# Kernel optimization log

Hardware: AMD Instinct MI355X
Metric: run time of the kernel (lower is better)

## Reference

```python
import jax, jax.numpy as jnp
import numpy as np

L_LAYERS = 4
D_MODEL = 512
NHEAD = 8
HEAD_DIM = D_MODEL // NHEAD  # 64
DFF = 2048
N_TGT = 1024
N_MEM = 2048
BATCH = 2
EPS = 1e-5


def setup_inputs() -> dict:
    key = jax.random.key(0)
    ks = jax.random.split(key, 16)
    sc = 0.02  # small init so deep residual stack stays numerically sane
    inp = dict(
        tgt=jax.random.normal(ks[0], (N_TGT, BATCH, D_MODEL), jnp.float32),
        memory=jax.random.normal(ks[1], (N_MEM, BATCH, D_MODEL), jnp.float32),
        query_pos=jax.random.normal(ks[2], (N_TGT, BATCH, D_MODEL), jnp.float32),
        pos=jax.random.normal(ks[3], (N_MEM, BATCH, D_MODEL), jnp.float32),
        # per-layer stacked parameters (leading axis = layer)
        in_proj_w=jax.random.normal(ks[4], (L_LAYERS, 3 * D_MODEL, D_MODEL), jnp.float32) * sc,
        in_proj_b=jnp.zeros((L_LAYERS, 3 * D_MODEL), jnp.float32),
        out_w=jax.random.normal(ks[5], (L_LAYERS, D_MODEL, D_MODEL), jnp.float32) * sc,
        out_b=jnp.zeros((L_LAYERS, D_MODEL), jnp.float32),
        conv_w=jax.random.normal(ks[6], (L_LAYERS, 3, D_MODEL, D_MODEL), jnp.float32) * sc,  # Conv1d k=1 == matmul
        conv_b=jnp.zeros((L_LAYERS, 3, D_MODEL), jnp.float32),
        mlp_w=jax.random.normal(ks[7], (L_LAYERS, 1, HEAD_DIM), jnp.float32) * sc,  # down_mlp Linear(head_dim,1)
        mlp_b=jnp.zeros((L_LAYERS, 1), jnp.float32),
        lin1_w=jax.random.normal(ks[8], (L_LAYERS, DFF, D_MODEL), jnp.float32) * sc,
        lin1_b=jnp.zeros((L_LAYERS, DFF), jnp.float32),
        lin2_w=jax.random.normal(ks[9], (L_LAYERS, D_MODEL, DFF), jnp.float32) * sc,
        lin2_b=jnp.zeros((L_LAYERS, D_MODEL), jnp.float32),
        ln_g=jnp.ones((L_LAYERS, 3, D_MODEL), jnp.float32),
        ln_b=jnp.zeros((L_LAYERS, 3, D_MODEL), jnp.float32),
        final_g=jnp.ones((D_MODEL,), jnp.float32),
        final_b=jnp.zeros((D_MODEL,), jnp.float32),
    )
    return inp


def _layer_norm(x, g, b):
    m = jnp.mean(x, axis=-1, keepdims=True)
    v = jnp.mean(jnp.square(x - m), axis=-1, keepdims=True)
    return (x - m) * jax.lax.rsqrt(v + EPS) * g + b


def _mha(q_in, k_in, v_in, w, b, ow, ob):
    # standard torch nn.MultiheadAttention, inputs [L, B, D]
    wq, wk, wv = jnp.split(w, 3, axis=0)
    bq, bk, bv = jnp.split(b, 3)

    def heads(x, W, bb):  # [L,B,D] -> [B,H,L,hd]
        y = x @ W.T + bb
        return y.reshape(y.shape[0], BATCH, NHEAD, HEAD_DIM).transpose(1, 2, 0, 3)

    qh = heads(q_in, wq, bq)
    kh = heads(k_in, wk, bk)
    vh = heads(v_in, wv, bv)
    scores = jnp.einsum('bhnd,bhmd->bhnm', qh, kh) / np.sqrt(HEAD_DIM).astype(np.float32)
    prob = jax.nn.softmax(scores, axis=-1)
    o = jnp.einsum('bhnm,bhmd->bhnd', prob, vh)
    o = o.transpose(2, 0, 1, 3).reshape(-1, BATCH, D_MODEL)  # [N,B,D]
    return o @ ow.T + ob


def _custom_attn(q_nbd, k_nbd, v_nbd, cw, cb, mw, mb):
    # MultiHeadedAttention: Conv1d(k=1) projections then key-modulated scores.
    def prep(x, W, bb):  # [L,B,D] -> [B, head_dim, H, L]  (reshape splits D into (head_dim, H))
        y = jnp.einsum('od,bdl->bol', W, x.transpose(1, 2, 0)) + bb[None, :, None]
        return y.reshape(BATCH, HEAD_DIM, NHEAD, -1)

    q = prep(q_nbd, cw[0], cb[0])  # [B,hd,H,N]
    k = prep(k_nbd, cw[1], cb[1])  # [B,hd,H,M]
    v = prep(v_nbd, cw[2], cb[2])  # [B,hd,H,M]
    # scores_1 = einsum('bdhn,bdhm->bhnm', q, k)/sqrt(hd); scores_2 = einsum('abcd,aced->abcd', k, scores_1)
    # = k[b,d,h,m] * sum_n scores_1[b,h,n,m]. Fuse the n-sum (same math, avoids [B,H,N,M]).
    s1sum = jnp.einsum('bdh,bdhm->bhm', q.sum(axis=3), k) / np.sqrt(HEAD_DIM).astype(np.float32)
    s2 = k * s1sum[:, None, :, :]            # [B,hd,H,M]
    prob = jax.nn.softmax(s2, axis=-1)       # softmax over M
    x = jnp.einsum('bnhm,bdhm->bdhn', prob, v)  # [B,hd,H,hd]
    x = jnp.einsum('bdhn,on->bdho', x, mw) + mb  # down_mlp -> [B,hd,H,1]
    return x.reshape(BATCH, D_MODEL, -1).transpose(2, 0, 1)  # [1,B,D], broadcasts on residual add


def _decoder_layer(tgt, memory, query_pos, pos, ipw, ipb, ow, ob, cw, cb, mw, mb,
                   l1w, l1b, l2w, l2b, lng, lnb):
    q = tgt + query_pos
    t2 = _mha(q, q, tgt, ipw, ipb, ow, ob)
    tgt = _layer_norm(tgt + t2, lng[0], lnb[0])
    t2 = _custom_attn(tgt + query_pos, memory + pos, memory, cw, cb, mw, mb)
    tgt = _layer_norm(tgt + t2, lng[1], lnb[1])
    h = jax.nn.relu(tgt @ l1w.T + l1b)
    t2 = h @ l2w.T + l2b
    tgt = _layer_norm(tgt + t2, lng[2], lnb[2])
    return tgt


def reference(tgt, memory, query_pos, pos, in_proj_w, in_proj_b, out_w, out_b,
              conv_w, conv_b, mlp_w, mlp_b, lin1_w, lin1_b, lin2_w, lin2_b,
              ln_g, ln_b, final_g, final_b):
    out = tgt
    for i in range(L_LAYERS):
        out = _decoder_layer(out, memory, query_pos, pos,
                             in_proj_w[i], in_proj_b[i], out_w[i], out_b[i],
                             conv_w[i], conv_b[i], mlp_w[i], mlp_b[i],
                             lin1_w[i], lin1_b[i], lin2_w[i], lin2_b[i],
                             ln_g[i], ln_b[i])
    out = _layer_norm(out, final_g, final_b)
    return out[None]  # Decoder returns output.unsqueeze(0): [1, N, B, D]
```

## Files before the change

kernel.cpp:

```cpp
#include <hip/hip_runtime.h>
#include <cstdint>

typedef __attribute__((ext_vector_type(8))) short short8;
typedef __attribute__((ext_vector_type(4))) float f32x4;
typedef __attribute__((ext_vector_type(4))) unsigned short us4;
typedef unsigned short u16;

static __device__ __forceinline__ u16 f2bf(float f) {
  union { float f; unsigned u; } x; x.f = f;
  return (u16)((x.u + 0x7FFFu + ((x.u >> 16) & 1u)) >> 16);
}

static __device__ __forceinline__ float wred_max(float v) {
#pragma unroll
  for (int o = 32; o > 0; o >>= 1) v = fmaxf(v, __shfl_xor(v, o, 64));
  return v;
}
static __device__ __forceinline__ float wred_sum(float v) {
#pragma unroll
  for (int o = 32; o > 0; o >>= 1) v += __shfl_xor(v, o, 64);
  return v;
}

static __device__ __forceinline__ void gload16(const void* g, void* l) {
  __builtin_amdgcn_global_load_lds(
      (const __attribute__((address_space(1))) unsigned int*)g,
      (__attribute__((address_space(3))) unsigned int*)l, 16, 0, 0);
}

struct GemmP {
  const u16* A; const u16* B; void* C; const float* bias;
  int M, N, K, lda, ldb, crs, ccs;
  int azi, bzi, czi, biasdz;
  long aso, asi, bso, bsi, cso, csi, biassz;
  float scale; int relu; int cbf16;
};

template<int ROWS>
static __device__ __forceinline__ void stage_t(const u16* g, int ld, u16* lds,
                                               int w, int lane) {
#pragma unroll
  for (int j = 0; j < ROWS / 32; ++j) {
    const int idx = w * (ROWS / 32) + j;
    const int r = idx * 8 + (lane >> 3);
    const int gc = ((lane & 7) ^ (r & 7)) * 8;
    gload16(g + (long)r * ld + gc, lds + idx * 512);
  }
}

template<int BM, int BN>
__global__ __launch_bounds__(256, 4) void gemm_k(GemmP p) {
  constexpr int WTM = BM / 2, WTN = BN / 2;
  constexpr int FM = WTM / 16, FN = WTN / 16;
  __shared__ __align__(16) u16 Al[2][BM * 64];
  __shared__ __align__(16) u16 Bl[2][BN * 64];
  const int tid = threadIdx.x, lane = tid & 63, w = tid >> 6;
  const int wr = w >> 1, wc = w & 1, lr = lane & 15, lk4 = lane >> 4;
  const int z = blockIdx.z;
  const int tm = blockIdx.y * BM, tn = blockIdx.x * BN;
  const long ab = (long)(z / p.azi) * p.aso + (long)(z % p.azi) * p.asi + (long)tm * p.lda;
  const long bb = (long)(z / p.bzi) * p.bso + (long)(z % p.bzi) * p.bsi + (long)tn * p.ldb;
  const long cb = (long)(z / p.czi) * p.cso + (long)(z % p.czi) * p.csi;
  const long boff = p.biasdz ? (long)(z / p.biasdz) * p.biassz : 0;

  f32x4 acc[FM][FN];
#pragma unroll
  for (int i = 0; i < FM; ++i)
#pragma unroll
    for (int j = 0; j < FN; ++j) acc[i][j] = (f32x4)(0.0f);

  const u16* Ag = p.A + ab;
  const u16* Bg = p.B + bb;
  stage_t<BM>(Ag, p.lda, &Al[0][0], w, lane);
  stage_t<BN>(Bg, p.ldb, &Bl[0][0], w, lane);
  __syncthreads();

  const int nt = p.K >> 6;
  for (int t = 0; t < nt; ++t) {
    const int cur = t & 1;
    if (t + 1 < nt) {
      stage_t<BM>(Ag + (long)(t + 1) * 64, p.lda, &Al[cur ^ 1][0], w, lane);
      stage_t<BN>(Bg + (long)(t + 1) * 64, p.ldb, &Bl[cur ^ 1][0], w, lane);
    }
    short8 af[FM][2], bfv[FN][2];
#pragma unroll
    for (int ks = 0; ks < 2; ++ks) {
#pragma unroll
      for (int mi = 0; mi < FM; ++mi) {
        const int row = wr * WTM + mi * 16 + lr;
        const int off = row * 128 + ((ks * 4 + lk4) ^ (row & 7)) * 16;
        af[mi][ks] = *(const short8*)((const char*)&Al[cur][0] + off);
      }
#pragma unroll
      for (int ni = 0; ni < FN; ++ni) {
        const int row = wc * WTN + ni * 16 + lr;
        const int off = row * 128 + ((ks * 4 + lk4) ^ (row & 7)) * 16;
        bfv[ni][ks] = *(const short8*)((const char*)&Bl[cur][0] + off);
      }
    }
#pragma unroll
    for (int ks = 0; ks < 2; ++ks)
#pragma unroll
      for (int mi = 0; mi < FM; ++mi)
#pragma unroll
        for (int ni = 0; ni < FN; ++ni)
          acc[mi][ni] = __builtin_amdgcn_mfma_f32_16x16x32_bf16(af[mi][ks], bfv[ni][ks],
                                                                acc[mi][ni], 0, 0, 0);
    __syncthreads();
  }

  const int kg = lk4 * 4;
#pragma unroll
  for (int ni = 0; ni < FN; ++ni) {
    const int col = tn + wc * WTN + ni * 16 + lr;
    const float bv = p.bias ? p.bias[boff + col] : 0.0f;
#pragma unroll
    for (int mi = 0; mi < FM; ++mi) {
      const int rb = tm + wr * WTM + mi * 16 + kg;
#pragma unroll
      for (int r = 0; r < 4; ++r) {
        float v = acc[mi][ni][r] * p.scale + bv;
        if (p.relu) v = fmaxf(v, 0.0f);
        const long ci = cb + (long)(rb + r) * p.crs + (long)col * p.ccs;
        if (p.cbf16) ((u16*)p.C)[ci] = f2bf(v);
        else ((float*)p.C)[ci] = v;
      }
    }
  }
}

template<int BM, int BN>
static inline void launchg(const GemmP& p, int nb, hipStream_t s) {
  dim3 g((unsigned)(p.N / BN), (unsigned)(p.M / BM), (unsigned)nb);
  hipLaunchKernelGGL((gemm_k<BM, BN>), g, dim3(256), 0, s, p);
}

__global__ __launch_bounds__(256) void flash_attn(const u16* qkb, const u16* Vtb, u16* aob) {
  const int zh = blockIdx.x, b = zh >> 3, h = zh & 7;
  const int qt = blockIdx.y;
  const int tid = threadIdx.x, lane = tid & 63, w = tid >> 6;
  const int lr = lane & 15, g = lane >> 4;

  __shared__ __align__(16) u16 Kl[2][64 * 64];
  __shared__ __align__(16) u16 Vl[2][64 * 64];
  __shared__ __align__(16) u16 Pl[4][16 * 64];

  const int nrow = qt * 64 + w * 16 + lr;
  const long qbase = ((long)(nrow * 2 + b)) * 1024 + h * 64;
  const short8 q0 = *(const short8*)&qkb[qbase + g * 8];
  const short8 q1 = *(const short8*)&qkb[qbase + 32 + g * 8];

  f32x4 acc_o[4];
#pragma unroll
  for (int i = 0; i < 4; ++i) acc_o[i] = (f32x4)(0.0f);
  float m_run = -3e38f, l_run = 0.0f;

  auto stage = [&](int buf, int t) {
    const int m0 = t * 64;
#pragma unroll
    for (int j = 0; j < 2; ++j) {
      const int c = w * 2 + j;
      const int row = c * 8 + (lane >> 3);
      const int src = (lane & 7) ^ (row & 7);
      gload16(qkb + ((long)((m0 + row) * 2 + b)) * 1024 + 512 + h * 64 + src * 8,
              &Kl[buf][c * 512]);
      gload16(Vtb + (long)b * 524288 + ((long)(h * 64 + row)) * 1024 + m0 + src * 8,
              &Vl[buf][c * 512]);
    }
  };

  stage(0, 0);
  __syncthreads();

  for (int t = 0; t < 16; ++t) {
    const int cur = t & 1;
    if (t < 15) stage(cur ^ 1, t + 1);

    f32x4 s_acc[4];
#pragma unroll
    for (int ks = 0; ks < 4; ++ks) {
      const int krow = ks * 16 + lr;
      const short8 k0 = *(const short8*)&Kl[cur][krow * 64 + ((g ^ (krow & 7)) * 8)];
      const short8 k1 = *(const short8*)&Kl[cur][krow * 64 + (((4 + g) ^ (krow & 7)) * 8)];
      f32x4 z4 = (f32x4)(0.0f);
      z4 = __builtin_amdgcn_mfma_f32_16x16x32_bf16(k0, q0, z4, 0, 0, 0);
      z4 = __builtin_amdgcn_mfma_f32_16x16x32_bf16(k1, q1, z4, 0, 0, 0);
      s_acc[ks] = z4;
    }

    float mx = -3e38f;
#pragma unroll
    for (int ks = 0; ks < 4; ++ks)
#pragma unroll
      for (int r = 0; r < 4; ++r) mx = fmaxf(mx, s_acc[ks][r]);
    mx = fmaxf(mx, __shfl_xor(mx, 16, 64));
    mx = fmaxf(mx, __shfl_xor(mx, 32, 64));
    mx *= 0.125f;
    const float m_new = fmaxf(m_run, mx);
    const float alpha = __expf(m_run - m_new);
    float psum = 0.0f;
    u16 pb[4][4];
#pragma unroll
    for (int ks = 0; ks < 4; ++ks)
#pragma unroll
      for (int r = 0; r < 4; ++r) {
        const float pv = __expf(s_acc[ks][r] * 0.125f - m_new);
        psum += pv;
        pb[ks][r] = f2bf(pv);
      }
    psum += __shfl_xor(psum, 16, 64);
    psum += __shfl_xor(psum, 32, 64);
    l_run = l_run * alpha + psum;
    m_run = m_new;
#pragma unroll
    for (int i = 0; i < 4; ++i) acc_o[i] *= alpha;

#pragma unroll
    for (int ks = 0; ks < 4; ++ks)
#pragma unroll
      for (int r = 0; r < 4; ++r) {
        const int m = ks * 16 + g * 4 + r;
        Pl[w][lr * 64 + (((m >> 3) ^ (lr & 7)) * 8) + (m & 7)] = pb[ks][r];
      }

#pragma unroll
    for (int mh = 0; mh < 2; ++mh) {
      const short8 pt = *(const short8*)&Pl[w][lr * 64 + (((mh * 4 + g) ^ (lr & 7)) * 8)];
#pragma unroll
      for (int ds = 0; ds < 4; ++ds) {
        const int drow = ds * 16 + lr;
        const short8 vt = *(const short8*)&Vl[cur][drow * 64 + (((mh * 4 + g) ^ (drow & 7)) * 8)];
        acc_o[ds] = __builtin_amdgcn_mfma_f32_16x16x32_bf16(vt, pt, acc_o[ds], 0, 0, 0);
      }
    }
    __syncthreads();
  }

  const float invl = 1.0f / l_run;
#pragma unroll
  for (int ds = 0; ds < 4; ++ds)
#pragma unroll
    for (int r = 0; r < 4; ++r) {
      const int d = ds * 16 + g * 4 + r;
      aob[((long)(nrow * 2 + b)) * 512 + h * 64 + d] = f2bf(acc_o[ds][r] * invl);
    }
}

__global__ __launch_bounds__(256) void ln512(const float* a, const float* res, int resmode,
                                             const float* g, const float* bt,
                                             float* out, u16* obf,
                                             const float* add2, u16* obf2) {
  const int row = blockIdx.x * 4 + (threadIdx.x >> 6);
  const int lane = threadIdx.x & 63;
  const float* ar = a + (long)row * 512;
  f32x4 x[2];
#pragma unroll
  for (int i = 0; i < 2; ++i) {
    const int idx = (i * 64 + lane) * 4;
    x[i] = *(const f32x4*)&ar[idx];
    if (resmode == 1) x[i] += *(const f32x4*)&res[(long)row * 512 + idx];
    else if (resmode == 2) x[i] += *(const f32x4*)&res[(row & 1) * 512 + idx];
  }
  float s = 0.f;
#pragma unroll
  for (int i = 0; i < 2; ++i)
#pragma unroll
    for (int j = 0; j < 4; ++j) s += x[i][j];
  const float mean = wred_sum(s) * (1.0f / 512.0f);
  float vv = 0.f;
#pragma unroll
  for (int i = 0; i < 2; ++i)
#pragma unroll
    for (int j = 0; j < 4; ++j) { const float d = x[i][j] - mean; vv += d * d; }
  vv = wred_sum(vv) * (1.0f / 512.0f);
  const float rs = rsqrtf(vv + 1e-5f);
#pragma unroll
  for (int i = 0; i < 2; ++i) {
    const int idx = (i * 64 + lane) * 4;
    const f32x4 gv = *(const f32x4*)&g[idx];
    const f32x4 bv = *(const f32x4*)&bt[idx];
    f32x4 o;
#pragma unroll
    for (int j = 0; j < 4; ++j) o[j] = (x[i][j] - mean) * rs * gv[j] + bv[j];
    *(f32x4*)&out[(long)row * 512 + idx] = o;
    if (obf) {
      us4 ov;
#pragma unroll
      for (int j = 0; j < 4; ++j) ov[j] = f2bf(o[j]);
      *(us4*)&obf[(long)row * 512 + idx] = ov;
    }
    if (obf2) {
      const f32x4 a2 = *(const f32x4*)&add2[(long)row * 512 + idx];
      us4 ov;
#pragma unroll
      for (int j = 0; j < 4; ++j) ov[j] = f2bf(o[j] + a2[j]);
      *(us4*)&obf2[(long)row * 512 + idx] = ov;
    }
  }
}

struct CvtSeg { const float* s; u16* d; int nblk; };
struct Cvt5 { CvtSeg seg[5]; };
__global__ __launch_bounds__(256) void cvt_multi(Cvt5 c) {
  int b = blockIdx.x, si = 0;
  while (si < 4 && b >= c.seg[si].nblk) { b -= c.seg[si].nblk; ++si; }
  const float* a = c.seg[si].s;
  u16* o = c.seg[si].d;
  const long i = ((long)b * 256 + threadIdx.x) * 8;
  f32x4 a0 = *(const f32x4*)&a[i], a1 = *(const f32x4*)&a[i + 4];
  short8 ov;
#pragma unroll
  for (int k = 0; k < 4; ++k) { ov[k] = (short)f2bf(a0[k]); ov[k + 4] = (short)f2bf(a1[k]); }
  *(short8*)&o[i] = ov;
}

__global__ __launch_bounds__(256) void cvt2(const float* a, const float* b, u16* oa, u16* oab) {
  const long i = ((long)blockIdx.x * 256 + threadIdx.x) * 8;
  f32x4 a0 = *(const f32x4*)&a[i], a1 = *(const f32x4*)&a[i + 4];
  f32x4 b0 = *(const f32x4*)&b[i], b1 = *(const f32x4*)&b[i + 4];
  short8 o1, o2;
#pragma unroll
  for (int c = 0; c < 4; ++c) {
    o1[c] = (short)f2bf(a0[c]); o1[c + 4] = (short)f2bf(a1[c]);
    o2[c] = (short)f2bf(a0[c] + b0[c]); o2[c + 4] = (short)f2bf(a1[c] + b1[c]);
  }
  *(short8*)&oa[i] = o1; *(short8*)&oab[i] = o2;
}

__global__ __launch_bounds__(512) void xsum1(const float* x1, const float* qpos, float* xp) {
  const int b = blockIdx.x >> 4, c = blockIdx.x & 15, d = threadIdx.x;
  float a = 0.f;
  for (int n = c * 64; n < c * 64 + 64; ++n) {
    const long i = ((long)(n * 2 + b)) * 512 + d;
    a += x1[i] + qpos[i];
  }
  xp[blockIdx.x * 512 + d] = a;
}

__global__ __launch_bounds__(512) void xsum2(const float* xp, float* xs) {
  const int b = blockIdx.x, d = threadIdx.x;
  float a = 0.f;
#pragma unroll
  for (int c = 0; c < 16; ++c) a += xp[(b * 16 + c) * 512 + d];
  xs[b * 512 + d] = a;
}

__global__ __launch_bounds__(256) void s1_k(const float* xs, const float* W0, const float* b0,
                                            const float* kT, float* s1) {
  const int z = blockIdx.x, b = z >> 3, h = z & 7;
  const int tid = threadIdx.x;
  __shared__ float part[4][64];
  __shared__ float qs[64];
  const int d = tid & 63, qd = tid >> 6;
  const int ch = d * 8 + h;
  float pp = 0.f;
  const float* wrp = W0 + (long)ch * 512 + qd * 128;
  const float* xrp = xs + b * 512 + qd * 128;
#pragma unroll 8
  for (int i = 0; i < 128; ++i) pp += wrp[i] * xrp[i];
  part[qd][d] = pp;
  __syncthreads();
  if (tid < 64)
    qs[tid] = part[0][tid] + part[1][tid] + part[2][tid] + part[3][tid]
              + 1024.0f * b0[tid * 8 + h];
  __syncthreads();
  const int m = blockIdx.y * 256 + tid;
  float a = 0.f;
#pragma unroll 8
  for (int dd = 0; dd < 64; ++dd)
    a += qs[dd] * kT[((long)b * 512 + dd * 8 + h) * 2048 + m];
  s1[(long)z * 2048 + m] = 0.125f * a;
}

__global__ __launch_bounds__(256) void pw_k(const float* kT, const float* s1,
                                            const float* mw, float* pwpart) {
  const int z = blockIdx.x & 15, c = blockIdx.x >> 4;
  const int b = z >> 3, h = z & 7;
  const int tid = threadIdx.x, lane = tid & 63, wid = tid >> 6;
  __shared__ float redm[4], reds[4];
  float s1v[8], pwa[8];
#pragma unroll
  for (int i = 0; i < 8; ++i) { s1v[i] = s1[(long)z * 2048 + tid + i * 256]; pwa[i] = 0.f; }
  for (int n = c * 8; n < c * 8 + 8; ++n) {
    const float* kr = kT + ((long)b * 512 + n * 8 + h) * 2048;
    float sv[8];
    float mx = -3e38f;
#pragma unroll
    for (int i = 0; i < 8; ++i) { sv[i] = kr[tid + i * 256] * s1v[i]; mx = fmaxf(mx, sv[i]); }
    mx = wred_max(mx);
    if (lane == 0) redm[wid] = mx;
    __syncthreads();
    mx = fmaxf(fmaxf(redm[0], redm[1]), fmaxf(redm[2], redm[3]));
    float sm = 0.f;
#pragma unroll
    for (int i = 0; i < 8; ++i) { sv[i] = __expf(sv[i] - mx); sm += sv[i]; }
    sm = wred_sum(sm);
    if (lane == 0) reds[wid] = sm;
    __syncthreads();
    sm = reds[0] + reds[1] + reds[2] + reds[3];
    const float wnl = mw[n] / sm;
#pragma unroll
    for (int i = 0; i < 8; ++i) pwa[i] += wnl * sv[i];
    __syncthreads();
  }
#pragma unroll
  for (int i = 0; i < 8; ++i)
    pwpart[((long)c * 16 + z) * 2048 + tid + i * 256] = pwa[i];
}

__global__ __launch_bounds__(256) void x2_k(const float* vT, const float* pwpart,
                                            const float* mb, float* t2c) {
  const int z = blockIdx.x, b = z >> 3, h = z & 7;
  const int tid = threadIdx.x, lane = tid & 63, wid = tid >> 6;
  float pwv[32];
#pragma unroll 4
  for (int i = 0; i < 32; ++i) {
    const int m = lane + i * 64;
    float s = 0.f;
#pragma unroll
    for (int c = 0; c < 8; ++c) s += pwpart[((long)c * 16 + z) * 2048 + m];
    pwv[i] = s;
  }
#pragma unroll
  for (int ci = 0; ci < 4; ++ci) {
    const int d = wid * 16 + blockIdx.y * 4 + ci, ch = d * 8 + h;
    const float* vr = vT + ((long)b * 512 + ch) * 2048;
    float acc = 0.f;
#pragma unroll 8
    for (int i = 0; i < 32; ++i) acc += vr[lane + i * 64] * pwv[i];
    acc = wred_sum(acc);
    if (lane == 0) t2c[b * 512 + ch] = acc + mb[0];
  }
}

extern "C" void kernel_launch(void* const* d_in, const int* in_sizes, int n_in,
                              void* d_out, int out_size, void* d_ws, size_t ws_size,
                              hipStream_t stream) {
  (void)in_sizes; (void)n_in; (void)out_size; (void)ws_size;
  const float* tgt   = (const float*)d_in[0];
  const float* memry = (const float*)d_in[1];
  const float* qpos  = (const float*)d_in[2];
  const float* pos   = (const float*)d_in[3];
  const float* ipw   = (const float*)d_in[4];
  const float* ipb   = (const float*)d_in[5];
  const float* outw  = (const float*)d_in[6];
  const float* outb  = (const float*)d_in[7];
  const float* convw = (const float*)d_in[8];
  const float* convb = (const float*)d_in[9];
  const float* mlpw  = (const float*)d_in[10];
  const float* mlpb  = (const float*)d_in[11];
  const float* l1w   = (const float*)d_in[12];
  const float* l1b   = (const float*)d_in[13];
  const float* l2w   = (const float*)d_in[14];
  const float* l2b   = (const float*)d_in[15];
  const float* lng   = (const float*)d_in[16];
  const float* lnbp  = (const float*)d_in[17];
  const float* fg    = (const float*)d_in[18];
  const float* fbv   = (const float*)d_in[19];

  char* base = (char*)d_ws;
  const long MBy = 1 << 20;
  u16*   qkb   = (u16*)(base + 0);
  u16*   Vtb   = (u16*)(base + 4 * MBy);
  u16*   aob   = (u16*)(base + 6 * MBy);
  u16*   xb    = (u16*)(base + 8 * MBy);
  u16*   xqb   = (u16*)(base + 10 * MBy);
  u16*   mempb = (u16*)(base + 12 * MBy);
  u16*   memb  = (u16*)(base + 16 * MBy);
  u16*   x2nb  = (u16*)(base + 20 * MBy);
  u16*   hb    = (u16*)(base + 22 * MBy);
  float* t2    = (float*)(base + 30 * MBy);
  float* x1    = (float*)(base + 34 * MBy);
  float* x2n   = (float*)(base + 38 * MBy);
  float* fbuf  = (float*)(base + 42 * MBy);
  float* xbuf  = (float*)(base + 46 * MBy);
  float* kT    = (float*)(base + 50 * MBy);
  float* vT    = (float*)(base + 58 * MBy);
  u16*   ipwb  = (u16*)(base + 66 * MBy);
  u16*   outwb = (u16*)(base + 72 * MBy);
  u16*   convwb= (u16*)(base + 74 * MBy);
  u16*   l1wb  = (u16*)(base + 80 * MBy);
  u16*   l2wb  = (u16*)(base + 88 * MBy);
  float* xpart = (float*)(base + 96 * MBy);
  float* xsumb = (float*)(base + 96 * MBy + 64 * 1024);
  float* s1b   = (float*)(base + 96 * MBy + 72 * 1024);
  float* pwpart= (float*)(base + 96 * MBy + 200 * 1024);
  float* t2c   = (float*)(base + 97 * MBy + 200 * 1024);

  {
    Cvt5 c;
    c.seg[0] = { ipw,   ipwb,  1536 };
    c.seg[1] = { outw,  outwb,  512 };
    c.seg[2] = { convw, convwb, 1536 };
    c.seg[3] = { l1w,   l1wb,  2048 };
    c.seg[4] = { l2w,   l2wb,  2048 };
    cvt_multi<<<dim3(7680), dim3(256), 0, stream>>>(c);
  }
  cvt2<<<dim3(1024), dim3(256), 0, stream>>>(memry, pos, memb, mempb);
  cvt2<<<dim3(512), dim3(256), 0, stream>>>(tgt, qpos, xb, xqb);

  for (int l = 0; l < 4; ++l) {
    const float* xin = l ? xbuf : tgt;

    GemmP p{};
    p.azi = p.bzi = p.czi = 1; p.scale = 1.0f;
    p.A = xqb; p.lda = 512; p.B = ipwb + (long)l * 786432; p.ldb = 512;
    p.C = qkb; p.crs = 1024; p.ccs = 1; p.cbf16 = 1;
    p.bias = ipb + (long)l * 1536;
    p.M = 2048; p.N = 1024; p.K = 512;
    launchg<64, 64>(p, 1, stream);

    p = GemmP{}; p.azi = p.bzi = p.czi = 1; p.scale = 1.0f;
    p.A = xb; p.lda = 1024; p.aso = 512;
    p.B = ipwb + (long)l * 786432 + 524288; p.ldb = 512;
    p.C = Vtb; p.crs = 1; p.ccs = 1024; p.cso = 524288; p.cbf16 = 1;
    p.bias = ipb + (long)l * 1536 + 1024;
    p.M = 1024; p.N = 512; p.K = 512;
    launchg<32, 64>(p, 2, stream);

    flash_attn<<<dim3(16, 16), dim3(256), 0, stream>>>(qkb, Vtb, aob);

    p = GemmP{}; p.azi = p.bzi = p.czi = 1; p.scale = 1.0f;
    p.A = aob; p.lda = 512; p.B = outwb + (long)l * 262144; p.ldb = 512;
    p.C = t2; p.crs = 512; p.ccs = 1; p.cbf16 = 0;
    p.bias = outb + l * 512;
    p.M = 2048; p.N = 512; p.K = 512;
    launchg<32, 64>(p, 1, stream);

    ln512<<<dim3(512), dim3(256), 0, stream>>>(t2, xin, 1, lng + (l * 3) * 512,
                                               lnbp + (l * 3) * 512, x1, nullptr,
                                               nullptr, nullptr);

    p = GemmP{}; p.scale = 1.0f;
    p.A = mempb; p.lda = 1024; p.azi = 2; p.aso = 2097152; p.asi = 512;
    p.B = convwb + ((long)l * 3 + 1) * 262144; p.ldb = 512;
    p.bzi = 2; p.bso = 262144; p.bsi = 0;
    p.C = kT; p.crs = 1; p.ccs = 2048;
    p.czi = 2; p.cso = 2097152; p.csi = 1048576; p.cbf16 = 0;
    p.bias = convb + (l * 3 + 1) * 512; p.biasdz = 2; p.biassz = 512;
    p.M = 2048; p.N = 512; p.K = 512;
    launchg<64, 64>(p, 4, stream);

    xsum1<<<dim3(32), dim3(512), 0, stream>>>(x1, qpos, xpart);
    xsum2<<<dim3(2), dim3(512), 0, stream>>>(xpart, xsumb);
    s1_k<<<dim3(16, 8), dim3(256), 0, stream>>>(xsumb, convw + ((long)l * 3) * 262144,
                                                convb + (l * 3) * 512, kT, s1b);
    pw_k<<<dim3(128), dim3(256), 0, stream>>>(kT, s1b, mlpw + l * 64, pwpart);
    x2_k<<<dim3(16, 4), dim3(256), 0, stream>>>(vT, pwpart, mlpb + l, t2c);

    ln512<<<dim3(512), dim3(256), 0, stream>>>(x1, t2c, 2, lng + (l * 3 + 1) * 512,
                                               lnbp + (l * 3 + 1) * 512, x2n, x2nb,
                                               nullptr, nullptr);

    p = GemmP{}; p.azi = p.bzi = p.czi = 1; p.scale = 1.0f;
    p.A = x2nb; p.lda = 512; p.B = l1wb + (long)l * 1048576; p.ldb = 512;
    p.C = hb; p.crs = 2048; p.ccs = 1; p.cbf16 = 1; p.relu = 1;
    p.bias = l1b + l * 2048;
    p.M = 2048; p.N = 2048; p.K = 512;
    launchg<64, 64>(p, 1, stream);

    p = GemmP{}; p.azi = p.bzi = p.czi = 1; p.scale = 1.0f;
    p.A = hb; p.lda = 2048; p.B = l2wb + (long)l * 1048576; p.ldb = 2048;
    p.C = fbuf; p.crs = 512; p.ccs = 1; p.cbf16 = 0;
    p.bias = l2b + l * 512;
    p.M = 2048; p.N = 512; p.K = 2048;
    launchg<32, 64>(p, 1, stream);

    ln512<<<dim3(512), dim3(256), 0, stream>>>(fbuf, x2n, 1, lng + (l * 3 + 2) * 512,
                                               lnbp + (l * 3 + 2) * 512, xbuf, xb,
                                               qpos, xqb);
  }
  ln512<<<dim3(512), dim3(256), 0, stream>>>(xbuf, nullptr, 0, fg, fbv,
                                             (float*)d_out, nullptr, nullptr, nullptr);
}
```

Baseline: 654.0 us.

## Batch conv K/V GEMMs upfront, fuse QK and V projections into one launch

```diff
diff --git a/kernel.cpp b/kernel.cpp
--- a/kernel.cpp
+++ b/kernel.cpp
@@ -30,10 +30,10 @@
 
 struct GemmP {
   const u16* A; const u16* B; void* C; const float* bias;
-  int M, N, K, lda, ldb, crs, ccs;
+  int K, lda, ldb, crs, ccs;
   int azi, bzi, czi, biasdz;
   long aso, asi, bso, bsi, cso, csi, biassz;
-  float scale; int relu; int cbf16;
+  float scale; int relu; int cbf16; int cm;
 };
 
 template<int ROWS>
@@ -49,15 +49,11 @@
 }
 
 template<int BM, int BN>
-__global__ __launch_bounds__(256, 4) void gemm_k(GemmP p) {
+static __device__ void gbody(const GemmP& p, int tm, int tn, int z, u16* Al, u16* Bl) {
   constexpr int WTM = BM / 2, WTN = BN / 2;
   constexpr int FM = WTM / 16, FN = WTN / 16;
-  __shared__ __align__(16) u16 Al[2][BM * 64];
-  __shared__ __align__(16) u16 Bl[2][BN * 64];
   const int tid = threadIdx.x, lane = tid & 63, w = tid >> 6;
   const int wr = w >> 1, wc = w & 1, lr = lane & 15, lk4 = lane >> 4;
-  const int z = blockIdx.z;
-  const int tm = blockIdx.y * BM, tn = blockIdx.x * BN;
   const long ab = (long)(z / p.azi) * p.aso + (long)(z % p.azi) * p.asi + (long)tm * p.lda;
   const long bb = (long)(z / p.bzi) * p.bso + (long)(z % p.bzi) * p.bsi + (long)tn * p.ldb;
   const long cb = (long)(z / p.czi) * p.cso + (long)(z % p.czi) * p.csi;
@@ -71,16 +67,16 @@
 
   const u16* Ag = p.A + ab;
   const u16* Bg = p.B + bb;
-  stage_t<BM>(Ag, p.lda, &Al[0][0], w, lane);
-  stage_t<BN>(Bg, p.ldb, &Bl[0][0], w, lane);
+  stage_t<BM>(Ag, p.lda, Al, w, lane);
+  stage_t<BN>(Bg, p.ldb, Bl, w, lane);
   __syncthreads();
 
   const int nt = p.K >> 6;
   for (int t = 0; t < nt; ++t) {
     const int cur = t & 1;
     if (t + 1 < nt) {
-      stage_t<BM>(Ag + (long)(t + 1) * 64, p.lda, &Al[cur ^ 1][0], w, lane);
-      stage_t<BN>(Bg + (long)(t + 1) * 64, p.ldb, &Bl[cur ^ 1][0], w, lane);
+      stage_t<BM>(Ag + (long)(t + 1) * 64, p.lda, Al + (cur ^ 1) * BM * 64, w, lane);
+      stage_t<BN>(Bg + (long)(t + 1) * 64, p.ldb, Bl + (cur ^ 1) * BN * 64, w, lane);
     }
     short8 af[FM][2], bfv[FN][2];
 #pragma unroll
@@ -89,13 +85,13 @@
       for (int mi = 0; mi < FM; ++mi) {
         const int row = wr * WTM + mi * 16 + lr;
         const int off = row * 128 + ((ks * 4 + lk4) ^ (row & 7)) * 16;
-        af[mi][ks] = *(const short8*)((const char*)&Al[cur][0] + off);
+        af[mi][ks] = *(const short8*)((const char*)(Al + cur * BM * 64) + off);
       }
 #pragma unroll
       for (int ni = 0; ni < FN; ++ni) {
         const int row = wc * WTN + ni * 16 + lr;
         const int off = row * 128 + ((ks * 4 + lk4) ^ (row & 7)) * 16;
-        bfv[ni][ks] = *(const short8*)((const char*)&Bl[cur][0] + off);
+        bfv[ni][ks] = *(const short8*)((const char*)(Bl + cur * BN * 64) + off);
       }
     }
 #pragma unroll
@@ -119,20 +115,51 @@
       const int rb = tm + wr * WTM + mi * 16 + kg;
 #pragma unroll
       for (int r = 0; r < 4; ++r) {
+        const int rw = rb + r;
         float v = acc[mi][ni][r] * p.scale + bv;
         if (p.relu) v = fmaxf(v, 0.0f);
-        const long ci = cb + (long)(rb + r) * p.crs + (long)col * p.ccs;
-        if (p.cbf16) ((u16*)p.C)[ci] = f2bf(v);
-        else ((float*)p.C)[ci] = v;
+        if (p.cm) {
+          const long ci = (long)(rw & 1) * 524288 + (long)col * 1024 + (rw >> 1);
+          ((u16*)p.C)[ci] = f2bf(v);
+        } else {
+          const long ci = cb + (long)rw * p.crs + (long)col * p.ccs;
+          if (p.cbf16) ((u16*)p.C)[ci] = f2bf(v);
+          else ((float*)p.C)[ci] = v;
+        }
       }
     }
   }
 }
 
 template<int BM, int BN>
-static inline void launchg(const GemmP& p, int nb, hipStream_t s) {
-  dim3 g((unsigned)(p.N / BN), (unsigned)(p.M / BM), (unsigned)nb);
-  hipLaunchKernelGGL((gemm_k<BM, BN>), g, dim3(256), 0, s, p);
+__global__ __launch_bounds__(256, 4) void gemm_k(GemmP p) {
+  __shared__ __align__(16) u16 Al[2 * BM * 64];
+  __shared__ __align__(16) u16 Bl[2 * BN * 64];
+  gbody<BM, BN>(p, blockIdx.y * BM, blockIdx.x * BN, blockIdx.z, Al, Bl);
+}
+
+__global__ __launch_bounds__(256, 4) void qkv2_k(GemmP q, GemmP v) {
+  __shared__ __align__(16) u16 Al[2 * 64 * 64];
+  __shared__ __align__(16) u16 Bl[2 * 64 * 64];
+  const int id = blockIdx.x;
+  if (id < 512) gbody<64, 64>(q, (id / 16) * 64, (id % 16) * 64, 0, Al, Bl);
+  else { const int u = id - 512; gbody<64, 64>(v, (u / 8) * 64, (u % 8) * 64, 0, Al, Bl); }
+}
+
+__global__ __launch_bounds__(256, 4) void convkv_k(const u16* mempb, const u16* convwb,
+                                                   const float* convb, float* kvall) {
+  __shared__ __align__(16) u16 Al[2 * 64 * 64];
+  __shared__ __align__(16) u16 Bl[2 * 64 * 64];
+  const int id = blockIdx.x;
+  const int z = id >> 8, rr = id & 255;
+  const int l = z >> 2, g = (z >> 1) & 1, b = z & 1;
+  GemmP p{};
+  p.A = mempb + g * 2097152 + b * 512; p.lda = 1024;
+  p.B = convwb + ((long)(l * 3 + 1 + g)) * 262144; p.ldb = 512;
+  p.C = kvall + (long)z * 1048576; p.crs = 1; p.ccs = 2048;
+  p.bias = convb + (l * 3 + 1 + g) * 512;
+  p.K = 512; p.azi = p.bzi = p.czi = 1; p.scale = 1.0f;
+  gbody<64, 64>(p, (rr >> 3) * 64, (rr & 7) * 64, 0, Al, Bl);
 }
 
 __global__ __launch_bounds__(256) void flash_attn(const u16* qkb, const u16* Vtb, u16* aob) {
@@ -155,7 +182,7 @@
   for (int i = 0; i < 4; ++i) acc_o[i] = (f32x4)(0.0f);
   float m_run = -3e38f, l_run = 0.0f;
 
-  auto stage = [&](int buf, int t) {
+  auto stg = [&](int buf, int t) {
     const int m0 = t * 64;
 #pragma unroll
     for (int j = 0; j < 2; ++j) {
@@ -169,12 +196,12 @@
     }
   };
 
-  stage(0, 0);
+  stg(0, 0);
   __syncthreads();
 
   for (int t = 0; t < 16; ++t) {
     const int cur = t & 1;
-    if (t < 15) stage(cur ^ 1, t + 1);
+    if (t < 15) stg(cur ^ 1, t + 1);
 
     f32x4 s_acc[4];
 #pragma unroll
@@ -327,48 +354,51 @@
   *(short8*)&oa[i] = o1; *(short8*)&oab[i] = o2;
 }
 
-__global__ __launch_bounds__(512) void xsum1(const float* x1, const float* qpos, float* xp) {
-  const int b = blockIdx.x >> 4, c = blockIdx.x & 15, d = threadIdx.x;
-  float a = 0.f;
-  for (int n = c * 64; n < c * 64 + 64; ++n) {
-    const long i = ((long)(n * 2 + b)) * 512 + d;
-    a += x1[i] + qpos[i];
-  }
-  xp[blockIdx.x * 512 + d] = a;
-}
-
-__global__ __launch_bounds__(512) void xsum2(const float* xp, float* xs) {
-  const int b = blockIdx.x, d = threadIdx.x;
-  float a = 0.f;
-#pragma unroll
-  for (int c = 0; c < 16; ++c) a += xp[(b * 16 + c) * 512 + d];
-  xs[b * 512 + d] = a;
-}
-
-__global__ __launch_bounds__(256) void s1_k(const float* xs, const float* W0, const float* b0,
+__global__ __launch_bounds__(256) void xsum1(const float* x1, const float* qpos, float* xp) {
+  const int u = blockIdx.x, b = u >> 5, c = u & 31, tid = threadIdx.x;
+  float a0 = 0.f, a1 = 0.f;
+  for (int n = c * 32; n < c * 32 + 32; ++n) {
+    const long i0 = ((long)(n * 2 + b)) * 512;
+    a0 += x1[i0 + tid] + qpos[i0 + tid];
+    a1 += x1[i0 + 256 + tid] + qpos[i0 + 256 + tid];
+  }
+  xp[(long)u * 512 + tid] = a0;
+  xp[(long)u * 512 + 256 + tid] = a1;
+}
+
+__global__ __launch_bounds__(256) void s1_k(const float* xp, const float* W0, const float* b0,
                                             const float* kT, float* s1) {
-  const int z = blockIdx.x, b = z >> 3, h = z & 7;
+  const int z = blockIdx.x, mc = blockIdx.y, b = z >> 3, h = z & 7;
   const int tid = threadIdx.x;
+  __shared__ float xsl[512];
   __shared__ float part[4][64];
-  __shared__ float qs[64];
-  const int d = tid & 63, qd = tid >> 6;
-  const int ch = d * 8 + h;
+  __shared__ float qsl[64];
+#pragma unroll
+  for (int dh = 0; dh < 2; ++dh) {
+    const int d = dh * 256 + tid;
+    float s = 0.f;
+#pragma unroll
+    for (int c = 0; c < 32; ++c) s += xp[((long)b * 32 + c) * 512 + d];
+    xsl[d] = s;
+  }
+  __syncthreads();
+  const int dd = tid & 63, qd = tid >> 6;
+  const int ch = dd * 8 + h;
   float pp = 0.f;
   const float* wrp = W0 + (long)ch * 512 + qd * 128;
-  const float* xrp = xs + b * 512 + qd * 128;
 #pragma unroll 8
-  for (int i = 0; i < 128; ++i) pp += wrp[i] * xrp[i];
-  part[qd][d] = pp;
+  for (int i = 0; i < 128; ++i) pp += wrp[i] * xsl[qd * 128 + i];
+  part[qd][dd] = pp;
   __syncthreads();
   if (tid < 64)
-    qs[tid] = part[0][tid] + part[1][tid] + part[2][tid] + part[3][tid]
-              + 1024.0f * b0[tid * 8 + h];
+    qsl[tid] = part[0][tid] + part[1][tid] + part[2][tid] + part[3][tid]
+               + 1024.0f * b0[tid * 8 + h];
   __syncthreads();
-  const int m = blockIdx.y * 256 + tid;
+  const int m = mc * 256 + tid;
   float a = 0.f;
 #pragma unroll 8
-  for (int dd = 0; dd < 64; ++dd)
-    a += qs[dd] * kT[((long)b * 512 + dd * 8 + h) * 2048 + m];
+  for (int d2 = 0; d2 < 64; ++d2)
+    a += qsl[d2] * kT[((long)b * 512 + d2 * 8 + h) * 2048 + m];
   s1[(long)z * 2048 + m] = 0.125f * a;
 }
 
@@ -474,18 +504,16 @@
   float* x2n   = (float*)(base + 38 * MBy);
   float* fbuf  = (float*)(base + 42 * MBy);
   float* xbuf  = (float*)(base + 46 * MBy);
-  float* kT    = (float*)(base + 50 * MBy);
-  float* vT    = (float*)(base + 58 * MBy);
-  u16*   ipwb  = (u16*)(base + 66 * MBy);
-  u16*   outwb = (u16*)(base + 72 * MBy);
-  u16*   convwb= (u16*)(base + 74 * MBy);
-  u16*   l1wb  = (u16*)(base + 80 * MBy);
-  u16*   l2wb  = (u16*)(base + 88 * MBy);
-  float* xpart = (float*)(base + 96 * MBy);
-  float* xsumb = (float*)(base + 96 * MBy + 64 * 1024);
-  float* s1b   = (float*)(base + 96 * MBy + 72 * 1024);
-  float* pwpart= (float*)(base + 96 * MBy + 200 * 1024);
-  float* t2c   = (float*)(base + 97 * MBy + 200 * 1024);
+  u16*   ipwb  = (u16*)(base + 50 * MBy);
+  u16*   outwb = (u16*)(base + 56 * MBy);
+  u16*   convwb= (u16*)(base + 58 * MBy);
+  u16*   l1wb  = (u16*)(base + 64 * MBy);
+  u16*   l2wb  = (u16*)(base + 72 * MBy);
+  float* xpart = (float*)(base + 80 * MBy);
+  float* s1b   = (float*)(base + 80 * MBy + 256 * 1024);
+  float* pwpart= (float*)(base + 81 * MBy);
+  float* t2c   = (float*)(base + 82 * MBy);
+  float* kvall = (float*)(base + 96 * MBy);
 
   {
     Cvt5 c;
@@ -498,74 +526,59 @@
   }
   cvt2<<<dim3(1024), dim3(256), 0, stream>>>(memry, pos, memb, mempb);
   cvt2<<<dim3(512), dim3(256), 0, stream>>>(tgt, qpos, xb, xqb);
+  convkv_k<<<dim3(4096), dim3(256), 0, stream>>>(mempb, convwb, convb, kvall);
 
   for (int l = 0; l < 4; ++l) {
     const float* xin = l ? xbuf : tgt;
-
-    GemmP p{};
-    p.azi = p.bzi = p.czi = 1; p.scale = 1.0f;
-    p.A = xqb; p.lda = 512; p.B = ipwb + (long)l * 786432; p.ldb = 512;
-    p.C = qkb; p.crs = 1024; p.ccs = 1; p.cbf16 = 1;
-    p.bias = ipb + (long)l * 1536;
-    p.M = 2048; p.N = 1024; p.K = 512;
-    launchg<64, 64>(p, 1, stream);
-
-    p = GemmP{}; p.azi = p.bzi = p.czi = 1; p.scale = 1.0f;
-    p.A = xb; p.lda = 1024; p.aso = 512;
-    p.B = ipwb + (long)l * 786432 + 524288; p.ldb = 512;
-    p.C = Vtb; p.crs = 1; p.ccs = 1024; p.cso = 524288; p.cbf16 = 1;
-    p.bias = ipb + (long)l * 1536 + 1024;
-    p.M = 1024; p.N = 512; p.K = 512;
-    launchg<32, 64>(p, 2, stream);
-
+    const float* kT = kvall + (long)l * 4194304;
+    const float* vT = kT + 2097152;
+
+    {
+      GemmP q{};
+      q.A = xqb; q.lda = 512; q.B = ipwb + (long)l * 786432; q.ldb = 512;
+      q.C = qkb; q.crs = 1024; q.ccs = 1; q.cbf16 = 1;
+      q.bias = ipb + (long)l * 1536;
+      q.K = 512; q.azi = q.bzi = q.czi = 1; q.scale = 1.0f;
+      GemmP v{};
+      v.A = xb; v.lda = 512; v.B = ipwb + (long)l * 786432 + 524288; v.ldb = 512;
+      v.C = Vtb; v.cm = 1; v.bias = ipb + (long)l * 1536 + 1024;
+      v.K = 512; v.azi = v.bzi = v.czi = 1; v.scale = 1.0f;
+      qkv2_k<<<dim3(768), dim3(256), 0, stream>>>(q, v);
+    }
     flash_attn<<<dim3(16, 16), dim3(256), 0, stream>>>(qkb, Vtb, aob);
-
-    p = GemmP{}; p.azi = p.bzi = p.czi = 1; p.scale = 1.0f;
-    p.A = aob; p.lda = 512; p.B = outwb + (long)l * 262144; p.ldb = 512;
-    p.C = t2; p.crs = 512; p.ccs = 1; p.cbf16 = 0;
-    p.bias = outb + l * 512;
-    p.M = 2048; p.N = 512; p.K = 512;
-    launchg<32, 64>(p, 1, stream);
-
+    {
+      GemmP o{};
+      o.A = aob; o.lda = 512; o.B = outwb + (long)l * 262144; o.ldb = 512;
+      o.C = t2; o.crs = 512; o.ccs = 1; o.bias = outb + l * 512;
+      o.K = 512; o.azi = o.bzi = o.czi = 1; o.scale = 1.0f;
+      gemm_k<32, 64><<<dim3(8, 64, 1), dim3(256), 0, stream>>>(o);
+    }
     ln512<<<dim3(512), dim3(256), 0, stream>>>(t2, xin, 1, lng + (l * 3) * 512,
                                                lnbp + (l * 3) * 512, x1, nullptr,
                                                nullptr, nullptr);
-
-    p = GemmP{}; p.scale = 1.0f;
-    p.A = mempb; p.lda = 1024; p.azi = 2; p.aso = 2097152; p.asi = 512;
-    p.B = convwb + ((long)l * 3 + 1) * 262144; p.ldb = 512;
-    p.bzi = 2; p.bso = 262144; p.bsi = 0;
-    p.C = kT; p.crs = 1; p.ccs = 2048;
-    p.czi = 2; p.cso = 2097152; p.csi = 1048576; p.cbf16 = 0;
-    p.bias = convb + (l * 3 + 1) * 512; p.biasdz = 2; p.biassz = 512;
-    p.M = 2048; p.N = 512; p.K = 512;
-    launchg<64, 64>(p, 4, stream);
-
-    xsum1<<<dim3(32), dim3(512), 0, stream>>>(x1, qpos, xpart);
-    xsum2<<<dim3(2), dim3(512), 0, stream>>>(xpart, xsumb);
-    s1_k<<<dim3(16, 8), dim3(256), 0, stream>>>(xsumb, convw + ((long)l * 3) * 262144,
+    xsum1<<<dim3(64), dim3(256), 0, stream>>>(x1, qpos, xpart);
+    s1_k<<<dim3(16, 8), dim3(256), 0, stream>>>(xpart, convw + ((long)l * 3) * 262144,
                                                 convb + (l * 3) * 512, kT, s1b);
     pw_k<<<dim3(128), dim3(256), 0, stream>>>(kT, s1b, mlpw + l * 64, pwpart);
     x2_k<<<dim3(16, 4), dim3(256), 0, stream>>>(vT, pwpart, mlpb + l, t2c);
-
     ln512<<<dim3(512), dim3(256), 0, stream>>>(x1, t2c, 2, lng + (l * 3 + 1) * 512,
                                                lnbp + (l * 3 + 1) * 512, x2n, x2nb,
                                                nullptr, nullptr);
-
-    p = GemmP{}; p.azi = p.bzi = p.czi = 1; p.scale = 1.0f;
-    p.A = x2nb; p.lda = 512; p.B = l1wb + (long)l * 1048576; p.ldb = 512;
-    p.C = hb; p.crs = 2048; p.ccs = 1; p.cbf16 = 1; p.relu = 1;
-    p.bias = l1b + l * 2048;
-    p.M = 2048; p.N = 2048; p.K = 512;
-    launchg<64, 64>(p, 1, stream);
-
-    p = GemmP{}; p.azi = p.bzi = p.czi = 1; p.scale = 1.0f;
-    p.A = hb; p.lda = 2048; p.B = l2wb + (long)l * 1048576; p.ldb = 2048;
-    p.C = fbuf; p.crs = 512; p.ccs = 1; p.cbf16 = 0;
-    p.bias = l2b + l * 512;
-    p.M = 2048; p.N = 512; p.K = 2048;
-    launchg<32, 64>(p, 1, stream);
-
+    {
+      GemmP f1{};
+      f1.A = x2nb; f1.lda = 512; f1.B = l1wb + (long)l * 1048576; f1.ldb = 512;
+      f1.C = hb; f1.crs = 2048; f1.ccs = 1; f1.cbf16 = 1; f1.relu = 1;
+      f1.bias = l1b + l * 2048;
+      f1.K = 512; f1.azi = f1.bzi = f1.czi = 1; f1.scale = 1.0f;
+      gemm_k<64, 64><<<dim3(32, 32, 1), dim3(256), 0, stream>>>(f1);
+    }
+    {
+      GemmP f2{};
+      f2.A = hb; f2.lda = 2048; f2.B = l2wb + (long)l * 1048576; f2.ldb = 2048;
+      f2.C = fbuf; f2.crs = 512; f2.ccs = 1; f2.bias = l2b + l * 512;
+      f2.K = 2048; f2.azi = f2.bzi = f2.czi = 1; f2.scale = 1.0f;
+      gemm_k<32, 64><<<dim3(8, 64, 1), dim3(256), 0, stream>>>(f2);
+    }
     ln512<<<dim3(512), dim3(256), 0, stream>>>(fbuf, x2n, 1, lng + (l * 3 + 2) * 512,
                                                lnbp + (l * 3 + 2) * 512, xbuf, xb,
                                                qpos, xqb);
```

After: 597.5 us. 8.6% less time.
